# Kernel tuning notes

Measured on AMD Instinct MI355X. Metric: run time of the kernel, lower is better.

## Reference

```python
import jax, jax.numpy as jnp
import numpy as np

B, NODES, D, DEG = 256, 124, 32, 16
N = B * NODES
EP = NODES * DEG
E = B * EP
L, H, C = 3, 4, 32
NCLS = 40
TMP = 124 + 32 * 2 * L
EPS = 1e-5
NEG_SLOPE = 0.2


def setup_inputs() -> dict:
    key = jax.random.key(0)
    ks = jax.random.split(key, 16)
    x = jax.random.normal(ks[0], (N, D), dtype=jnp.float32)
    # per-graph random edges, guaranteed no self-loops
    src = jax.random.randint(ks[1], (B, EP), 0, NODES)
    off = jax.random.randint(ks[2], (B, EP), 1, NODES)
    dst = (src + off) % NODES
    goff = (jnp.arange(B) * NODES)[:, None]
    edge_index = jnp.stack([(src + goff).reshape(-1), (dst + goff).reshape(-1)]).astype(jnp.int32)
    batch = jnp.repeat(jnp.arange(B), NODES).astype(jnp.int32)
    conv_W = jax.random.normal(ks[3], (L, D, H * C), dtype=jnp.float32) / np.sqrt(D)
    conv_att_l = jax.random.normal(ks[4], (L, H, C), dtype=jnp.float32) * 0.1
    conv_att_r = jax.random.normal(ks[5], (L, H, C), dtype=jnp.float32) * 0.1
    conv_bias = jnp.zeros((L, C), dtype=jnp.float32)
    bn_gamma = jnp.ones((L, C), dtype=jnp.float32)
    bn_beta = jnp.zeros((L, C), dtype=jnp.float32)
    lin1_W = jax.random.normal(ks[6], (NODES * C, 124), dtype=jnp.float32) / np.sqrt(NODES * C)
    lin1_b = jnp.zeros((124,), dtype=jnp.float32)
    bn1_gamma = jnp.ones((124,), dtype=jnp.float32)
    bn1_beta = jnp.zeros((124,), dtype=jnp.float32)
    lin2_W = jax.random.normal(ks[7], (TMP, NCLS), dtype=jnp.float32) / np.sqrt(TMP)
    lin2_b = jnp.zeros((NCLS,), dtype=jnp.float32)
    return dict(x=x, edge_index=edge_index, batch=batch, conv_W=conv_W,
                conv_att_l=conv_att_l, conv_att_r=conv_att_r, conv_bias=conv_bias,
                bn_gamma=bn_gamma, bn_beta=bn_beta, lin1_W=lin1_W, lin1_b=lin1_b,
                bn1_gamma=bn1_gamma, bn1_beta=bn1_beta, lin2_W=lin2_W, lin2_b=lin2_b)


def _supergat_mx(x, src, dst, W, att_l, att_r, bias):
    # SuperGATConv, attention_type='MX', concat=False (mean over heads), eval mode
    h = (x @ W).reshape(N, H, C)              # [N,H,C]
    x_j = h[src]                              # source / message features [E',H,C]
    x_i = h[dst]                              # target features
    logits = jnp.sum(x_i * x_j, -1)           # [E',H] dot-product logits
    alpha = jnp.sum(x_j * att_l, -1) + jnp.sum(x_i * att_r, -1)
    alpha = alpha * jax.nn.sigmoid(logits)
    alpha = jax.nn.leaky_relu(alpha, NEG_SLOPE)
    # scatter-softmax over incoming edges of each target node
    amax = jax.ops.segment_max(alpha, dst, num_segments=N)
    ex = jnp.exp(alpha - amax[dst])
    denom = jax.ops.segment_sum(ex, dst, num_segments=N)
    a = ex / (denom[dst] + 1e-16)             # [E',H]
    out = jax.ops.segment_sum(x_j * a[..., None], dst, num_segments=N)  # [N,H,C]
    return out.mean(axis=1) + bias            # concat=False -> head mean, [N,C]


def _batchnorm(x, gamma, beta):
    mu = x.mean(0)
    var = x.var(0)
    return (x - mu) * jax.lax.rsqrt(var + EPS) * gamma + beta


def reference(x, edge_index, batch, conv_W, conv_att_l, conv_att_r, conv_bias,
              bn_gamma, bn_beta, lin1_W, lin1_b, bn1_gamma, bn1_beta, lin2_W, lin2_b):
    # add self loops once (input edges contain none)
    sl = jnp.arange(N, dtype=edge_index.dtype)
    src = jnp.concatenate([edge_index[0], sl])
    dst = jnp.concatenate([edge_index[1], sl])
    inter = []
    for l in range(L):
        x = _supergat_mx(x, src, dst, conv_W[l], conv_att_l[l], conv_att_r[l], conv_bias[l])
        x = _batchnorm(x, bn_gamma[l], bn_beta[l])
        x = jax.nn.relu(x)
        cnt = jax.ops.segment_sum(jnp.ones((N,), x.dtype), batch, num_segments=B)
        gmean = jax.ops.segment_sum(x, batch, num_segments=B) / cnt[:, None]
        gmax = jax.ops.segment_max(x, batch, num_segments=B)
        inter.append(jnp.concatenate([gmean, gmax], 1))   # [B, 2C]
    x = x.reshape(B, NODES * C)
    x = x @ lin1_W + lin1_b
    x = _batchnorm(x, bn1_gamma, bn1_beta)
    x = jnp.concatenate([x] + inter, 1)                   # inter_connect=True
    x = jax.nn.relu(x)
    return x @ lin2_W + lin2_b                            # [B, NCLS]
```

## Files before the change

### kernel.cpp

```cpp
#include <hip/hip_runtime.h>
#include <math.h>

#define NN 31744
#define NE 507904
#define EP 1984
#define NODES 124
#define NB 256
#define CC 32
#define HC 128
#define FEAT_DIM 316
#define NCLS 40
#define NC 3968
#define EXCAP 192

typedef __attribute__((ext_vector_type(8))) short bf16x8;
typedef __attribute__((ext_vector_type(4))) float f32x4;

#define LOG2E  1.44269504f
#define LOG2E5 0.28853901f

__device__ __forceinline__ unsigned short f2bf(float f) {
    unsigned u = __float_as_uint(f);
    u = u + 0x7FFFu + ((u >> 16) & 1u);
    return (unsigned short)(u >> 16);
}
__device__ __forceinline__ float bf2f(unsigned short s) {
    return __uint_as_float(((unsigned)s) << 16);
}

__global__ __launch_bounds__(256) void mask_build(const int* __restrict__ ei,
                                                  unsigned* __restrict__ gmask,
                                                  int* __restrict__ gdst,
                                                  int* __restrict__ gdent,
                                                  float* __restrict__ bnacc) {
    __shared__ unsigned mcnt[NODES * NODES];
    __shared__ int cnt[128], pref[128];
    __shared__ int locs[124][8];
    int g = blockIdx.x, t = threadIdx.x;
    if (g == 0 && t < 192) bnacc[t] = 0.f;
    for (int i = t; i < NODES * NODES; i += 256) mcnt[i] = 0u;
    __syncthreads();
    for (int e = t; e < EP; e += 256) {
        int s = ei[g * EP + e] - g * NODES;
        int d = ei[NE + g * EP + e] - g * NODES;
        atomicAdd(&mcnt[d * NODES + s], 1u);
    }
    __syncthreads();
    int nd = 0;
    if (t < 124) {
        unsigned m[4] = {0u, 0u, 0u, 0u};
        for (int s = 0; s < NODES; ++s) {
            unsigned c = mcnt[t * NODES + s] + (s == t ? 1u : 0u);
            if (c) {
                m[s >> 5] |= 1u << (s & 31);
                if (c > 1u && nd < 8) { locs[t][nd] = (s << 8) | (int)c; nd++; }
            }
        }
        uint4 mm; mm.x = m[0]; mm.y = m[1]; mm.z = m[2]; mm.w = m[3];
        *(uint4*)&gmask[(size_t)(g * NODES + t) * 4] = mm;
        cnt[t] = nd;
    } else if (t < 128) cnt[t] = 0;
    __syncthreads();
    if (t < 128) pref[t] = cnt[t];
    __syncthreads();
    for (int off = 1; off < 128; off <<= 1) {
        int v = (t >= off && t < 128) ? pref[t - off] : 0;
        __syncthreads();
        if (t < 128) pref[t] += v;
        __syncthreads();
    }
    if (t < 124) {
        int off = pref[t] - cnt[t];
        gdst[g * 132 + t] = off < EXCAP ? off : EXCAP;
        for (int j = 0; j < nd; ++j)
            if (off + j < EXCAP) gdent[g * EXCAP + off + j] = locs[t][j];
    }
    if (t == 0) {
        int tot = pref[127];
        gdst[g * 132 + 124] = tot < EXCAP ? tot : EXCAP;
    }
}

__global__ __launch_bounds__(256) void wtrans(const float* __restrict__ W,
                                              unsigned short* __restrict__ WT) {
    __shared__ float tile[32][33];
    int kb = blockIdx.x, jb = blockIdx.y;
    int t = threadIdx.x;
    int tr = t >> 5, tc = t & 31;
    for (int r = tr; r < 32; r += 8) {
        int k = kb * 32 + r, j = jb * 32 + tc;
        tile[r][tc] = (j < 124) ? W[k * 124 + j] : 0.f;
    }
    __syncthreads();
    for (int r = tr; r < 32; r += 8) {
        int j = jb * 32 + r, k = kb * 32 + tc;
        WT[(size_t)j * NC + k] = f2bf(tile[tc][r]);
    }
}

#define HS 136
#define TS 136
#define XS 40
#define ABS 136
#define PWS 40

__global__ __launch_bounds__(1024, 1) void conv_graph(
    const float* __restrict__ xin, const float* __restrict__ W,
    const float* __restrict__ attl, const float* __restrict__ attr,
    const float* __restrict__ bias,
    const unsigned* __restrict__ gmask, const int* __restrict__ gdst,
    const int* __restrict__ gdent,
    const float* __restrict__ bnprev, const float* __restrict__ gprev,
    const float* __restrict__ bprev, float* __restrict__ feat, int lprev,
    float* __restrict__ y, float* __restrict__ bnacc) {

    __shared__ short hbh[128 * HS];
    __shared__ short hbl[128 * HS];
    __shared__ short hTall[128 * TS];
    __shared__ short pwbuf[16 * 1280];
    __shared__ short attBuf[16 * ABS];
    __shared__ float ALs[4][128], ARs[4][128];
    __shared__ unsigned mask[128][4];
    __shared__ unsigned short dupst[136];
    __shared__ unsigned dupent[EXCAP];
    __shared__ float bias_s[32];
    __shared__ float bsum[8][32], bsq[8][32];
    __shared__ float pmean[32];
    __shared__ int pmax[32];

    int g = blockIdx.x, t = threadIdx.x, base = g * NODES;
    short* xh  = pwbuf;
    short* xl  = pwbuf + 5120;
    short* WTh = hTall;
    short* WTl = hTall + 5120;

    if (t < 32) { pmean[t] = 0.f; pmax[t] = 0; }
    __syncthreads();

    {
        const float4* xsrc = (const float4*)(xin + (size_t)base * CC);
        for (int i = t; i < 992; i += 1024) {
            float4 v = xsrc[i];
            int n = i >> 3, c4 = i & 7;
            if (lprev >= 0) {
                float vv[4] = {v.x, v.y, v.z, v.w};
#pragma unroll
                for (int q = 0; q < 4; ++q) {
                    int c = c4 * 4 + q;
                    float mu = bnprev[c] * (1.f / NN);
                    float var = bnprev[32 + c] * (1.f / NN) - mu * mu;
                    float sc = rsqrtf(var + 1e-5f) * gprev[c];
                    float xv = (vv[q] - mu) * sc + bprev[c];
                    xv = fmaxf(xv, 0.f);
                    vv[q] = xv;
                    atomicAdd(&pmean[c], xv);
                    atomicMax(&pmax[c], __float_as_int(xv));
                }
                v.x = vv[0]; v.y = vv[1]; v.z = vv[2]; v.w = vv[3];
            }
            unsigned short h0 = f2bf(v.x), h1 = f2bf(v.y), h2 = f2bf(v.z), h3 = f2bf(v.w);
            unsigned short l0 = f2bf(v.x - bf2f(h0)), l1 = f2bf(v.y - bf2f(h1));
            unsigned short l2 = f2bf(v.z - bf2f(h2)), l3 = f2bf(v.w - bf2f(h3));
            uint2 ph; ph.x = ((unsigned)h1 << 16) | h0; ph.y = ((unsigned)h3 << 16) | h2;
            uint2 pl; pl.x = ((unsigned)l1 << 16) | l0; pl.y = ((unsigned)l3 << 16) | l2;
            *(uint2*)&xh[n * XS + c4 * 4] = ph;
            *(uint2*)&xl[n * XS + c4 * 4] = pl;
        }
        if (t < 4 * XS) { xh[124 * XS + t] = 0; xl[124 * XS + t] = 0; }
    }
    {
        int hc = t & 127, mq = t >> 7, ks = mq * 4;
        unsigned short hh4[4], ll4[4];
#pragma unroll
        for (int q = 0; q < 4; ++q) {
            float w = W[(ks + q) * HC + hc];
            hh4[q] = f2bf(w);
            ll4[q] = f2bf(w - bf2f(hh4[q]));
        }
        uint2 ph; ph.x = ((unsigned)hh4[1] << 16) | hh4[0]; ph.y = ((unsigned)hh4[3] << 16) | hh4[2];
        uint2 pl; pl.x = ((unsigned)ll4[1] << 16) | ll4[0]; pl.y = ((unsigned)ll4[3] << 16) | ll4[2];
        *(uint2*)&WTh[hc * XS + ks] = ph;
        *(uint2*)&WTl[hc * XS + ks] = pl;
    }
    for (int i = t; i < 2048; i += 1024) {
        int n = i >> 7, k = i & 127;
        float v = 0.f;
        int hidx = n & 3;
        if (n < 8 && (k >> 5) == hidx)
            v = (n < 4) ? attl[hidx * 32 + (k & 31)] : attr[hidx * 32 + (k & 31)];
        attBuf[n * ABS + k] = (short)f2bf(v);
    }
    if (t < CC) bias_s[t] = bias[t];
    if (t < 128) {
        if (t < 124) {
            uint4 m = *(const uint4*)&gmask[(size_t)(base + t) * 4];
            mask[t][0] = m.x; mask[t][1] = m.y; mask[t][2] = m.z; mask[t][3] = m.w;
        } else { mask[t][0] = 0u; mask[t][1] = 0u; mask[t][2] = 0u; mask[t][3] = 0u; }
    }
    if (t < 136) dupst[t] = (unsigned short)gdst[g * 132 + (t < 124 ? t : 124)];
    if (t >= 832 && t < 832 + EXCAP) dupent[t - 832] = (unsigned)gdent[g * EXCAP + (t - 832)];
    __syncthreads();

    if (lprev >= 0 && t < 32) {
        float* fp = feat + g * FEAT_DIM + NODES + lprev * 64;
        fp[t] = pmean[t] * (1.f / NODES);
        fp[32 + t] = __int_as_float(pmax[t]);
    }

    int wv = t >> 6, l = t & 63;
    int l15 = l & 15, l4 = l >> 4;

#pragma unroll
    for (int j = 0; j < 4; ++j) {
        int idx = wv * 4 + j;
        int tr = idx >> 3, tc = idx & 7;
        bf16x8 ah = *(bf16x8*)&xh[(tr * 16 + l15) * XS + l4 * 8];
        bf16x8 al_ = *(bf16x8*)&xl[(tr * 16 + l15) * XS + l4 * 8];
        bf16x8 bh = *(bf16x8*)&WTh[(tc * 16 + l15) * XS + l4 * 8];
        bf16x8 bl_ = *(bf16x8*)&WTl[(tc * 16 + l15) * XS + l4 * 8];
        f32x4 z = {0.f, 0.f, 0.f, 0.f};
        f32x4 c0 = __builtin_amdgcn_mfma_f32_16x16x32_bf16(ah, bh, z, 0, 0, 0);
        f32x4 c1 = __builtin_amdgcn_mfma_f32_16x16x32_bf16(ah, bl_, z, 0, 0, 0);
        f32x4 c2 = __builtin_amdgcn_mfma_f32_16x16x32_bf16(al_, bh, z, 0, 0, 0);
        f32x4 c = (c0 + c1) + c2;
        int hc = tc * 16 + l15;
#pragma unroll
        for (int r = 0; r < 4; ++r) {
            int n = tr * 16 + l4 * 4 + r;
            float s = c[r];
            unsigned short hi = f2bf(s);
            hbh[n * HS + hc] = (short)hi;
            hbl[n * HS + hc] = (short)f2bf(s - bf2f(hi));
        }
    }
    __syncthreads();

    if (wv < 8) {
        f32x4 c = {0.f, 0.f, 0.f, 0.f};
#pragma unroll
        for (int kb = 0; kb < 4; ++kb) {
            bf16x8 a = *(bf16x8*)&hbh[(wv * 16 + l15) * HS + kb * 32 + l4 * 8];
            bf16x8 b = *(bf16x8*)&attBuf[l15 * ABS + kb * 32 + l4 * 8];
            c = __builtin_amdgcn_mfma_f32_16x16x32_bf16(a, b, c, 0, 0, 0);
        }
        if (l15 < 8) {
#pragma unroll
            for (int r = 0; r < 4; ++r) {
                int n = wv * 16 + l4 * 4 + r;
                if (l15 < 4) ALs[l15][n] = c[r];
                else         ARs[l15 - 4][n] = c[r];
            }
        }
    }
#pragma unroll
    for (int hh2 = 0; hh2 < 4; ++hh2) {
        int k = t & 31, n4 = t >> 5;
        unsigned short r4[4];
#pragma unroll
        for (int r = 0; r < 4; ++r)
            r4[r] = (unsigned short)hbh[(n4 * 4 + r) * HS + hh2 * 32 + k];
        uint2 pk;
        pk.x = ((unsigned)r4[1] << 16) | r4[0];
        pk.y = ((unsigned)r4[3] << 16) | r4[2];
        *(uint2*)&hTall[(hh2 * 32 + k) * TS + n4 * 4] = pk;
    }
    __syncthreads();

    int DJ = wv >> 1;
    float accA[4] = {0.f, 0.f, 0.f, 0.f};
    float accB[4] = {0.f, 0.f, 0.f, 0.f};
    {
        int hh0 = (wv & 1) * 2;
        short* pwb = pwbuf + wv * 1280;
        int dst = DJ * 16 + l15;
        uint4 mrow = *(uint4*)&mask[dst][0];
        unsigned mwords[4] = {mrow.x, mrow.y, mrow.z, mrow.w};
        unsigned cntp[8];
#pragma unroll
        for (int SI = 0; SI < 8; ++SI) {
            unsigned mw = (mwords[SI >> 1] >> ((SI & 1) * 16 + l4 * 4)) & 0xFu;
            cntp[SI] = (mw & 1u) | ((mw & 2u) << 7) | ((mw & 4u) << 14) | ((mw & 8u) << 21);
        }
        {
            int s0 = dupst[dst], s1 = dupst[dst + 1];
            for (int e = s0; e < s1; ++e) {
                unsigned ent = dupent[e];
                unsigned src = (ent >> 8) & 255u;
                unsigned SI = src >> 4;
                unsigned r = (src & 15u) - (unsigned)(l4 * 4);
                if (r < 4u) {
                    unsigned sh = 8u * r;
                    cntp[SI] = (cntp[SI] & ~(255u << sh)) | ((ent & 255u) << sh);
                }
            }
        }

#define GRAM(kb, slot) { \
    _Pragma("unroll") \
    for (int s2 = 0; s2 < 2; ++s2) { \
        int SI = (kb) * 2 + s2; \
        int ao = (SI * 16 + l15) * HS + hh * 32 + l4 * 8; \
        bf16x8 ah = *(bf16x8*)&hbh[ao]; \
        bf16x8 al_ = *(bf16x8*)&hbl[ao]; \
        f32x4 z2 = {0.f, 0.f, 0.f, 0.f}; \
        f32x4 c0 = __builtin_amdgcn_mfma_f32_16x16x32_bf16(ah, gb, z2, 0, 0, 0); \
        f32x4 c1 = __builtin_amdgcn_mfma_f32_16x16x32_bf16(ah, gl, z2, 0, 0, 0); \
        f32x4 c2 = __builtin_amdgcn_mfma_f32_16x16x32_bf16(al_, gb, z2, 0, 0, 0); \
        f32x4 c = (c0 + c1) + c2; \
        int src0 = SI * 16 + l4 * 4; \
        float4 al4 = *(float4*)&ALs[hh][src0]; \
        unsigned cp = cntp[SI]; \
        float pv[4]; \
        _Pragma("unroll") \
        for (int r = 0; r < 4; ++r) { \
            float e2 = __builtin_amdgcn_exp2f(-LOG2E * c[r]); \
            float sig = __builtin_amdgcn_rcpf(1.f + e2); \
            float a2 = (((const float*)&al4)[r] + ar) * sig; \
            float m = fmaxf(a2 * LOG2E, a2 * LOG2E5); \
            float cr = (float)((cp >> (8 * r)) & 255u); \
            pv[r] = __builtin_amdgcn_exp2f(m) * cr; \
        } \
        sden += (pv[0] + pv[1]) + (pv[2] + pv[3]); \
        unsigned w0_, w1_; \
        asm("v_cvt_pk_bf16_f32 %0, %1, %2" : "=v"(w0_) : "v"(pv[0]), "v"(pv[1])); \
        asm("v_cvt_pk_bf16_f32 %0, %1, %2" : "=v"(w1_) : "v"(pv[2]), "v"(pv[3])); \
        uint2 pk_; pk_.x = w0_; pk_.y = w1_; \
        *(uint2*)&pwb[(slot) * 640 + l15 * PWS + s2 * 16 + l4 * 4] = pk_; \
    } }

#define PVOP(kb, slot) { \
    bf16x8 a = *(bf16x8*)&pwb[(slot) * 640 + l15 * PWS + l4 * 8]; \
    bf16x8 b0 = *(bf16x8*)&hTall[(hh * 32 + l15) * TS + (kb) * 32 + l4 * 8]; \
    bf16x8 b1 = *(bf16x8*)&hTall[(hh * 32 + 16 + l15) * TS + (kb) * 32 + l4 * 8]; \
    num0 = __builtin_amdgcn_mfma_f32_16x16x32_bf16(a, b0, num0, 0, 0, 0); \
    num1 = __builtin_amdgcn_mfma_f32_16x16x32_bf16(a, b1, num1, 0, 0, 0); }

#pragma unroll
        for (int jj = 0; jj < 2; ++jj) {
            int hh = hh0 + jj;
            bf16x8 gb = *(bf16x8*)&hbh[dst * HS + hh * 32 + l4 * 8];
            bf16x8 gl = *(bf16x8*)&hbl[dst * HS + hh * 32 + l4 * 8];
            float ar = ARs[hh][dst];
            float sden = 0.f;
            f32x4 num0 = {0.f, 0.f, 0.f, 0.f};
            f32x4 num1 = {0.f, 0.f, 0.f, 0.f};
            GRAM(0, 0);
            GRAM(1, 1); PVOP(0, 0);
            GRAM(2, 0); PVOP(1, 1);
            GRAM(3, 1); PVOP(2, 0);
            PVOP(3, 1);
            sden += __shfl_xor(sden, 16, 64);
            sden += __shfl_xor(sden, 32, 64);
#pragma unroll
            for (int r = 0; r < 4; ++r) {
                float dn = __shfl(sden, l4 * 4 + r, 64) + 1e-16f;
                accA[r] += ((float*)&num0)[r] / dn;
                accB[r] += ((float*)&num1)[r] / dn;
            }
        }
#undef GRAM
#undef PVOP
    }
    __syncthreads();

    float* exch = (float*)pwbuf;
    if (wv & 1) {
#pragma unroll
        for (int r = 0; r < 4; ++r) {
            exch[DJ * 512 + l15 * 16 + l4 * 4 + r] = accA[r];
            exch[DJ * 512 + 256 + l15 * 16 + l4 * 4 + r] = accB[r];
        }
    }
    __syncthreads();

    if (!(wv & 1)) {
        float sA = 0.f, qA = 0.f, sB = 0.f, qB = 0.f;
#pragma unroll
        for (int r = 0; r < 4; ++r) {
            int n = DJ * 16 + l4 * 4 + r;
            float a = accA[r] + exch[DJ * 512 + l15 * 16 + l4 * 4 + r];
            float b = accB[r] + exch[DJ * 512 + 256 + l15 * 16 + l4 * 4 + r];
            a = 0.25f * a + bias_s[l15];
            b = 0.25f * b + bias_s[16 + l15];
            if (n < NODES) {
                y[(size_t)(base + n) * CC + l15] = a;
                y[(size_t)(base + n) * CC + 16 + l15] = b;
                sA += a; qA += a * a; sB += b; qB += b * b;
            }
        }
        sA += __shfl_xor(sA, 16, 64); sA += __shfl_xor(sA, 32, 64);
        qA += __shfl_xor(qA, 16, 64); qA += __shfl_xor(qA, 32, 64);
        sB += __shfl_xor(sB, 16, 64); sB += __shfl_xor(sB, 32, 64);
        qB += __shfl_xor(qB, 16, 64); qB += __shfl_xor(qB, 32, 64);
        if (l < 16) {
            bsum[DJ][l15] = sA; bsum[DJ][16 + l15] = sB;
            bsq[DJ][l15] = qA;  bsq[DJ][16 + l15] = qB;
        }
    }
    __syncthreads();
    if (t < CC) {
        float S = 0.f, Q = 0.f;
#pragma unroll
        for (int w = 0; w < 8; ++w) { S += bsum[w][t]; Q += bsq[w][t]; }
        atomicAdd(&bnacc[t], S);
        atomicAdd(&bnacc[CC + t], Q);
    }
}

__global__ void bn_relu_pool(const float* __restrict__ y, const float* __restrict__ acc,
                             const float* __restrict__ gamma, const float* __restrict__ beta,
                             unsigned short* __restrict__ xbf, float* __restrict__ feat, int l) {
    int g = blockIdx.x;
    int t = threadIdx.x;
    int c = t & 31, r0 = t >> 5;
    float mu = acc[c] * (1.f / NN);
    float var = acc[32 + c] * (1.f / NN) - mu * mu;
    float sc = rsqrtf(var + 1e-5f) * gamma[c];
    float bt = beta[c];
    float s = 0.f, mx = -INFINITY;
    for (int r = r0; r < NODES; r += 4) {
        int i = (g * NODES + r) * CC + c;
        float v = (y[i] - mu) * sc + bt;
        v = fmaxf(v, 0.f);
        xbf[i] = f2bf(v);
        s += v; mx = fmaxf(mx, v);
    }
    __shared__ float ls[128], lm[128];
    ls[t] = s; lm[t] = mx;
    __syncthreads();
    if (t < 32) {
        float S = ls[t] + ls[32 + t] + ls[64 + t] + ls[96 + t];
        float M = fmaxf(fmaxf(lm[t], lm[32 + t]), fmaxf(lm[64 + t], lm[96 + t]));
        float* fp = feat + g * FEAT_DIM + NODES + l * 64;
        fp[t] = S * (1.f / NODES);
        fp[32 + t] = M;
    }
}

#define L1_KS 4
#define L1_KC 992
#define XP 1000
__global__ __launch_bounds__(512) void lin1_mfma(const unsigned short* __restrict__ Xb,
                                                 const unsigned short* __restrict__ WT,
                                                 float* __restrict__ part) {
    __shared__ unsigned short Xs[16 * XP];
    int mt = blockIdx.x >> 2, kp = blockIdx.x & 3;
    int t = threadIdx.x;
    int wv = t >> 6, l = t & 63, l15 = l & 15, l4 = l >> 4;
    int M0 = mt * 16, k0 = kp * L1_KC;
    for (int i = t; i < 16 * 124; i += 512) {
        int r = i / 124, c = i - r * 124;
        *(uint4*)&Xs[r * XP + c * 8] = *(const uint4*)&Xb[(size_t)(M0 + r) * NC + k0 + c * 8];
    }
    __syncthreads();
    int N0 = wv * 16;
    f32x4 acc = {0.f, 0.f, 0.f, 0.f};
#pragma unroll 4
    for (int kk = 0; kk < 31; ++kk) {
        bf16x8 a = *(bf16x8*)&Xs[l15 * XP + kk * 32 + l4 * 8];
        bf16x8 b = *(const bf16x8*)&WT[(size_t)(N0 + l15) * NC + k0 + kk * 32 + l4 * 8];
        acc = __builtin_amdgcn_mfma_f32_16x16x32_bf16(a, b, acc, 0, 0, 0);
    }
    if (N0 + l15 < 124) {
#pragma unroll
        for (int r = 0; r < 4; ++r)
            part[(size_t)kp * NB * 124 + (M0 + l4 * 4 + r) * 124 + N0 + l15] = acc[r];
    }
}

__global__ void lin1_reduce(const float* __restrict__ part, const float* __restrict__ b,
                            float* __restrict__ out1) {
    int i = blockIdx.x * blockDim.x + threadIdx.x;
    if (i >= NB * 124) return;
    int j = i % 124;
    float s = b[j];
#pragma unroll
    for (int ks = 0; ks < L1_KS; ++ks) s += part[ks * NB * 124 + i];
    out1[i] = s;
}

__global__ void bn1_relu(const float* __restrict__ out1, const float* __restrict__ gamma,
                         const float* __restrict__ beta, float* __restrict__ feat) {
    __shared__ float ps[4][124], pq[4][124], smu[124], ssc[124], sbt[124];
    int t = threadIdx.x;
    int c = t & 127, seg = t >> 7;
    float s = 0.f, q = 0.f;
    if (c < 124) {
        for (int b = seg * 64; b < seg * 64 + 64; ++b) {
            float v = out1[b * 124 + c]; s += v; q += v * v;
        }
        ps[seg][c] = s; pq[seg][c] = q;
    }
    __syncthreads();
    if (t < 124) {
        float S = ps[0][t] + ps[1][t] + ps[2][t] + ps[3][t];
        float Q = pq[0][t] + pq[1][t] + pq[2][t] + pq[3][t];
        float mu = S * (1.f / NB);
        float var = Q * (1.f / NB) - mu * mu;
        smu[t] = mu; ssc[t] = rsqrtf(var + 1e-5f) * gamma[t]; sbt[t] = beta[t];
    }
    __syncthreads();
    if (c < 124) {
        for (int b = seg * 64; b < seg * 64 + 64; ++b) {
            float v = (out1[b * 124 + c] - smu[c]) * ssc[c] + sbt[c];
            feat[b * FEAT_DIM + c] = fmaxf(v, 0.f);
        }
    }
}

__global__ void lin2_k(const float* __restrict__ feat, const float* __restrict__ W,
                       const float* __restrict__ b, float* __restrict__ out) {
    __shared__ float psum[8][40];
    int g = blockIdx.x;
    int t = threadIdx.x;
    int j = t % 40, u = t / 40;
    if (u < 8) {
        int k0 = u * 40, k1 = (u == 7) ? FEAT_DIM : k0 + 40;
        float s = 0.f;
        for (int k = k0; k < k1; ++k) s += feat[g * FEAT_DIM + k] * W[k * NCLS + j];
        psum[u][j] = s;
    }
    __syncthreads();
    if (t < NCLS) {
        float s = b[t];
#pragma unroll
        for (int u2 = 0; u2 < 8; ++u2) s += psum[u2][t];
        out[g * NCLS + t] = s;
    }
}

extern "C" void kernel_launch(void* const* d_in, const int* in_sizes, int n_in,
                              void* d_out, int out_size, void* d_ws, size_t ws_size,
                              hipStream_t stream) {
    const float* x      = (const float*)d_in[0];
    const int*   ei     = (const int*)d_in[1];
    const float* conv_W = (const float*)d_in[3];
    const float* att_l  = (const float*)d_in[4];
    const float* att_r  = (const float*)d_in[5];
    const float* conv_b = (const float*)d_in[6];
    const float* bn_g   = (const float*)d_in[7];
    const float* bn_b   = (const float*)d_in[8];
    const float* lin1_W = (const float*)d_in[9];
    const float* lin1_b = (const float*)d_in[10];
    const float* bn1_g  = (const float*)d_in[11];
    const float* bn1_b  = (const float*)d_in[12];
    const float* lin2_W = (const float*)d_in[13];
    const float* lin2_b = (const float*)d_in[14];

    float* ws = (float*)d_ws;
    float* y = ws;
    unsigned short* xbf = (unsigned short*)(y + (size_t)NN * CC);
    float* bnacc = (float*)(xbf + (size_t)NN * CC);
    float* feat  = bnacc + 192;
    float* out1  = feat + NB * FEAT_DIM;
    float* part  = out1 + NB * 124;
    unsigned short* WT = (unsigned short*)(part + L1_KS * NB * 124);
    unsigned* gmask = (unsigned*)(WT + (size_t)128 * NC);
    int* gdst  = (int*)(gmask + (size_t)NN * 4);
    int* gdent = gdst + NB * 132;

    mask_build<<<NB, 256, 0, stream>>>(ei, gmask, gdst, gdent, bnacc);
    wtrans<<<dim3(NC / 32, 4), 256, 0, stream>>>(lin1_W, WT);

    const float* xin = x;
    for (int l = 0; l < 3; ++l) {
        const float* bnprev = (l == 0) ? nullptr : bnacc + (l - 1) * 64;
        const float* gprev  = (l == 0) ? bn_g : bn_g + (l - 1) * CC;
        const float* bprev  = (l == 0) ? bn_b : bn_b + (l - 1) * CC;
        conv_graph<<<NB, 1024, 0, stream>>>(xin, conv_W + l * CC * HC,
                                            att_l + l * HC, att_r + l * HC,
                                            conv_b + l * CC, gmask, gdst, gdent,
                                            bnprev, gprev, bprev, feat, l - 1,
                                            y, bnacc + l * 64);
        xin = y;
    }

    bn_relu_pool<<<NB, 128, 0, stream>>>(y, bnacc + 128, bn_g + 2 * CC, bn_b + 2 * CC,
                                         xbf, feat, 2);
    lin1_mfma<<<64, 512, 0, stream>>>(xbf, WT, part);
    lin1_reduce<<<(NB * 124 + 255) / 256, 256, 0, stream>>>(part, lin1_b, out1);
    bn1_relu<<<1, 512, 0, stream>>>(out1, bn1_g, bn1_b, feat);
    lin2_k<<<NB, 320, 0, stream>>>(feat, lin2_W, lin2_b, (float*)d_out);
}
```

Before: 145.6 us.

## Interleave two heads in attention MFMA pipeline and fuse lin1 reduce into BN1

The conv attention loop now processes both heads of a wave together, interleaving Gram/softmax MFMAs of one head with P·V MFMAs of the other so the two dependency chains can overlap. This gives more independent work per issue slot, at the cost of extra live registers for the second head's accumulators and operands. Separately, the split-K partial sum reduction for lin1 is folded into the single-block BN1 kernel, which removes one kernel launch. The trade-off is that the reduction now runs inside a single block instead of a grid-wide kernel, and it hardcodes four K-splits.

```diff
diff --git a/kernel.cpp b/kernel.cpp
--- a/kernel.cpp
+++ b/kernel.cpp
@@ -271,6 +271,7 @@
     float accB[4] = {0.f, 0.f, 0.f, 0.f};
     {
         int hh0 = (wv & 1) * 2;
+        int hh1 = hh0 + 1;
         short* pwb = pwbuf + wv * 1280;
         int dst = DJ * 16 + l15;
         uint4 mrow = *(uint4*)&mask[dst][0];
@@ -294,18 +295,27 @@
                 }
             }
         }
-
-#define GRAM(kb, slot) { \
+        bf16x8 gb0 = *(bf16x8*)&hbh[dst * HS + hh0 * 32 + l4 * 8];
+        bf16x8 gl0 = *(bf16x8*)&hbl[dst * HS + hh0 * 32 + l4 * 8];
+        bf16x8 gb1 = *(bf16x8*)&hbh[dst * HS + hh1 * 32 + l4 * 8];
+        bf16x8 gl1 = *(bf16x8*)&hbl[dst * HS + hh1 * 32 + l4 * 8];
+        float ar0 = ARs[hh0][dst];
+        float ar1 = ARs[hh1][dst];
+        float sden0 = 0.f, sden1 = 0.f;
+        f32x4 numA0 = {0.f, 0.f, 0.f, 0.f}, numB0 = {0.f, 0.f, 0.f, 0.f};
+        f32x4 numA1 = {0.f, 0.f, 0.f, 0.f}, numB1 = {0.f, 0.f, 0.f, 0.f};
+
+#define GRAMX(hh, gbv, glv, arv, sdenv, kb, slot) { \
     _Pragma("unroll") \
     for (int s2 = 0; s2 < 2; ++s2) { \
         int SI = (kb) * 2 + s2; \
-        int ao = (SI * 16 + l15) * HS + hh * 32 + l4 * 8; \
+        int ao = (SI * 16 + l15) * HS + (hh) * 32 + l4 * 8; \
         bf16x8 ah = *(bf16x8*)&hbh[ao]; \
         bf16x8 al_ = *(bf16x8*)&hbl[ao]; \
         f32x4 z2 = {0.f, 0.f, 0.f, 0.f}; \
-        f32x4 c0 = __builtin_amdgcn_mfma_f32_16x16x32_bf16(ah, gb, z2, 0, 0, 0); \
-        f32x4 c1 = __builtin_amdgcn_mfma_f32_16x16x32_bf16(ah, gl, z2, 0, 0, 0); \
-        f32x4 c2 = __builtin_amdgcn_mfma_f32_16x16x32_bf16(al_, gb, z2, 0, 0, 0); \
+        f32x4 c0 = __builtin_amdgcn_mfma_f32_16x16x32_bf16(ah, gbv, z2, 0, 0, 0); \
+        f32x4 c1 = __builtin_amdgcn_mfma_f32_16x16x32_bf16(ah, glv, z2, 0, 0, 0); \
+        f32x4 c2 = __builtin_amdgcn_mfma_f32_16x16x32_bf16(al_, gbv, z2, 0, 0, 0); \
         f32x4 c = (c0 + c1) + c2; \
         int src0 = SI * 16 + l4 * 4; \
         float4 al4 = *(float4*)&ALs[hh][src0]; \
@@ -315,12 +325,12 @@
         for (int r = 0; r < 4; ++r) { \
             float e2 = __builtin_amdgcn_exp2f(-LOG2E * c[r]); \
             float sig = __builtin_amdgcn_rcpf(1.f + e2); \
-            float a2 = (((const float*)&al4)[r] + ar) * sig; \
+            float a2 = (((const float*)&al4)[r] + (arv)) * sig; \
             float m = fmaxf(a2 * LOG2E, a2 * LOG2E5); \
             float cr = (float)((cp >> (8 * r)) & 255u); \
             pv[r] = __builtin_amdgcn_exp2f(m) * cr; \
         } \
-        sden += (pv[0] + pv[1]) + (pv[2] + pv[3]); \
+        sdenv += (pv[0] + pv[1]) + (pv[2] + pv[3]); \
         unsigned w0_, w1_; \
         asm("v_cvt_pk_bf16_f32 %0, %1, %2" : "=v"(w0_) : "v"(pv[0]), "v"(pv[1])); \
         asm("v_cvt_pk_bf16_f32 %0, %1, %2" : "=v"(w1_) : "v"(pv[2]), "v"(pv[3])); \
@@ -328,38 +338,41 @@
         *(uint2*)&pwb[(slot) * 640 + l15 * PWS + s2 * 16 + l4 * 4] = pk_; \
     } }
 
-#define PVOP(kb, slot) { \
+#define PVX(hh, numAv, numBv, kb, slot) { \
     bf16x8 a = *(bf16x8*)&pwb[(slot) * 640 + l15 * PWS + l4 * 8]; \
-    bf16x8 b0 = *(bf16x8*)&hTall[(hh * 32 + l15) * TS + (kb) * 32 + l4 * 8]; \
-    bf16x8 b1 = *(bf16x8*)&hTall[(hh * 32 + 16 + l15) * TS + (kb) * 32 + l4 * 8]; \
-    num0 = __builtin_amdgcn_mfma_f32_16x16x32_bf16(a, b0, num0, 0, 0, 0); \
-    num1 = __builtin_amdgcn_mfma_f32_16x16x32_bf16(a, b1, num1, 0, 0, 0); }
-
-#pragma unroll
-        for (int jj = 0; jj < 2; ++jj) {
-            int hh = hh0 + jj;
-            bf16x8 gb = *(bf16x8*)&hbh[dst * HS + hh * 32 + l4 * 8];
-            bf16x8 gl = *(bf16x8*)&hbl[dst * HS + hh * 32 + l4 * 8];
-            float ar = ARs[hh][dst];
-            float sden = 0.f;
-            f32x4 num0 = {0.f, 0.f, 0.f, 0.f};
-            f32x4 num1 = {0.f, 0.f, 0.f, 0.f};
-            GRAM(0, 0);
-            GRAM(1, 1); PVOP(0, 0);
-            GRAM(2, 0); PVOP(1, 1);
-            GRAM(3, 1); PVOP(2, 0);
-            PVOP(3, 1);
-            sden += __shfl_xor(sden, 16, 64);
-            sden += __shfl_xor(sden, 32, 64);
-#pragma unroll
-            for (int r = 0; r < 4; ++r) {
-                float dn = __shfl(sden, l4 * 4 + r, 64) + 1e-16f;
-                accA[r] += ((float*)&num0)[r] / dn;
-                accB[r] += ((float*)&num1)[r] / dn;
-            }
-        }
-#undef GRAM
-#undef PVOP
+    bf16x8 b0 = *(bf16x8*)&hTall[((hh) * 32 + l15) * TS + (kb) * 32 + l4 * 8]; \
+    bf16x8 b1 = *(bf16x8*)&hTall[((hh) * 32 + 16 + l15) * TS + (kb) * 32 + l4 * 8]; \
+    numAv = __builtin_amdgcn_mfma_f32_16x16x32_bf16(a, b0, numAv, 0, 0, 0); \
+    numBv = __builtin_amdgcn_mfma_f32_16x16x32_bf16(a, b1, numBv, 0, 0, 0); }
+
+        GRAMX(hh0, gb0, gl0, ar0, sden0, 0, 0);
+        GRAMX(hh1, gb1, gl1, ar1, sden1, 0, 1);
+        PVX(hh0, numA0, numB0, 0, 0);
+        GRAMX(hh0, gb0, gl0, ar0, sden0, 1, 0);
+        PVX(hh1, numA1, numB1, 0, 1);
+        GRAMX(hh1, gb1, gl1, ar1, sden1, 1, 1);
+        PVX(hh0, numA0, numB0, 1, 0);
+        GRAMX(hh0, gb0, gl0, ar0, sden0, 2, 0);
+        PVX(hh1, numA1, numB1, 1, 1);
+        GRAMX(hh1, gb1, gl1, ar1, sden1, 2, 1);
+        PVX(hh0, numA0, numB0, 2, 0);
+        GRAMX(hh0, gb0, gl0, ar0, sden0, 3, 0);
+        PVX(hh1, numA1, numB1, 2, 1);
+        GRAMX(hh1, gb1, gl1, ar1, sden1, 3, 1);
+        PVX(hh0, numA0, numB0, 3, 0);
+        PVX(hh1, numA1, numB1, 3, 1);
+#undef GRAMX
+#undef PVX
+
+        sden0 += __shfl_xor(sden0, 16, 64); sden0 += __shfl_xor(sden0, 32, 64);
+        sden1 += __shfl_xor(sden1, 16, 64); sden1 += __shfl_xor(sden1, 32, 64);
+#pragma unroll
+        for (int r = 0; r < 4; ++r) {
+            float dn0 = __shfl(sden0, l4 * 4 + r, 64) + 1e-16f;
+            float dn1 = __shfl(sden1, l4 * 4 + r, 64) + 1e-16f;
+            accA[r] = ((float*)&numA0)[r] / dn0 + ((float*)&numA1)[r] / dn1;
+            accB[r] = ((float*)&numB0)[r] / dn0 + ((float*)&numB1)[r] / dn1;
+        }
     }
     __syncthreads();
 
@@ -468,26 +481,24 @@
     }
 }
 
-__global__ void lin1_reduce(const float* __restrict__ part, const float* __restrict__ b,
-                            float* __restrict__ out1) {
-    int i = blockIdx.x * blockDim.x + threadIdx.x;
-    if (i >= NB * 124) return;
-    int j = i % 124;
-    float s = b[j];
-#pragma unroll
-    for (int ks = 0; ks < L1_KS; ++ks) s += part[ks * NB * 124 + i];
-    out1[i] = s;
-}
-
-__global__ void bn1_relu(const float* __restrict__ out1, const float* __restrict__ gamma,
-                         const float* __restrict__ beta, float* __restrict__ feat) {
+__global__ __launch_bounds__(512) void bn1_fused(const float* __restrict__ part,
+                                                 const float* __restrict__ b,
+                                                 const float* __restrict__ gamma,
+                                                 const float* __restrict__ beta,
+                                                 float* __restrict__ out1,
+                                                 float* __restrict__ feat) {
     __shared__ float ps[4][124], pq[4][124], smu[124], ssc[124], sbt[124];
     int t = threadIdx.x;
     int c = t & 127, seg = t >> 7;
     float s = 0.f, q = 0.f;
     if (c < 124) {
-        for (int b = seg * 64; b < seg * 64 + 64; ++b) {
-            float v = out1[b * 124 + c]; s += v; q += v * v;
+        float bb = b[c];
+        for (int r = seg * 64; r < seg * 64 + 64; ++r) {
+            int i = r * 124 + c;
+            float v = bb + part[i] + part[NB * 124 + i]
+                    + part[2 * NB * 124 + i] + part[3 * NB * 124 + i];
+            out1[i] = v;
+            s += v; q += v * v;
         }
         ps[seg][c] = s; pq[seg][c] = q;
     }
@@ -501,9 +512,9 @@
     }
     __syncthreads();
     if (c < 124) {
-        for (int b = seg * 64; b < seg * 64 + 64; ++b) {
-            float v = (out1[b * 124 + c] - smu[c]) * ssc[c] + sbt[c];
-            feat[b * FEAT_DIM + c] = fmaxf(v, 0.f);
+        for (int r = seg * 64; r < seg * 64 + 64; ++r) {
+            float v = (out1[r * 124 + c] - smu[c]) * ssc[c] + sbt[c];
+            feat[r * FEAT_DIM + c] = fmaxf(v, 0.f);
         }
     }
 }
@@ -578,7 +589,6 @@
     bn_relu_pool<<<NB, 128, 0, stream>>>(y, bnacc + 128, bn_g + 2 * CC, bn_b + 2 * CC,
                                          xbf, feat, 2);
     lin1_mfma<<<64, 512, 0, stream>>>(xbf, WT, part);
-    lin1_reduce<<<(NB * 124 + 255) / 256, 256, 0, stream>>>(part, lin1_b, out1);
-    bn1_relu<<<1, 512, 0, stream>>>(out1, bn1_g, bn1_b, feat);
+    bn1_fused<<<1, 512, 0, stream>>>(part, lin1_b, bn1_g, bn1_b, out1, feat);
     lin2_k<<<NB, 320, 0, stream>>>(feat, lin2_W, lin2_b, (float*)d_out);
 }
```

Measured after the change: 156.1 us. 1.07x slower.
